# Kernel tuning notes

Hardware: AMD Instinct MI355X
Metric: run time of the kernel (lower is better)

## Reference

```python
import jax, jax.numpy as jnp
import numpy as np
from jax.scipy.special import gammaln

# ---- constants matching init_kwargs ----
D = 64            # num_nodes
K = 64            # DiBS latent rank (k = d default)
P = 32            # n_particles
N_MC = 16         # MC graph samples for score-function grad estimator
PROJ = 128        # proj_dims
N = 2048          # observations
H = 5.0           # h_latent (Frobenius squared-exponential kernel bandwidth)
ALPHA = 0.2       # alpha_linear * t  (single SVGD step)
STEP = 0.005      # SVGD step size
ALPHA_MU = 1.0
ALPHA_LAMBD = float(D + 2)
THETA_MU = 0.0
P_EDGE = 4.0 / (D - 1)          # Erdos-Renyi edge prob (~2 expected edges/node)
LATENT_STD = 1.0 / np.sqrt(K)   # DiBS default latent prior std


def bge_log_marginal(g, data, mu0, alpha_mu, alpha_lambd):
    """BGe log marginal likelihood log p(data | G) for 0/1 adjacency g [d,d]."""
    n, d = data.shape
    small_t = alpha_mu * (alpha_lambd - d - 1.0) / (alpha_mu + 1.0)
    xbar = data.mean(0)
    xc = data - xbar
    R = small_t * jnp.eye(d) + xc.T @ xc \
        + (n * alpha_mu / (n + alpha_mu)) * jnp.outer(xbar - mu0, xbar - mu0)

    def masked_slogdet(mask):  # logdet of R restricted to mask-selected rows/cols
        m = jnp.outer(mask, mask)
        return jnp.linalg.slogdet(m * R + (1.0 - m) * jnp.eye(d))[1]

    def node_score(j):
        parents = g[:, j].astype(R.dtype)
        pj = jnp.maximum(parents, (jnp.arange(d) == j).astype(R.dtype))
        l = jnp.sum(parents)
        log_gamma = (0.5 * (jnp.log(alpha_mu) - jnp.log(n + alpha_mu))
                     + gammaln(0.5 * (n + alpha_lambd - d + l + 1.0))
                     - gammaln(0.5 * (alpha_lambd - d + l + 1.0))
                     - 0.5 * n * jnp.log(jnp.pi)
                     + 0.5 * (alpha_lambd - d + 2.0 * l + 1.0) * jnp.log(small_t))
        return (log_gamma
                + 0.5 * (n + alpha_lambd - d + l) * masked_slogdet(parents)
                - 0.5 * (n + alpha_lambd - d + l + 1.0) * masked_slogdet(pj))

    return jnp.sum(jax.vmap(node_score)(jnp.arange(d)))


def _dense(key, fan_in, fan_out):
    return jax.random.normal(key, (fan_in, fan_out), jnp.float32) * 0.05


def setup_inputs() -> dict:
    key = jax.random.key(0)
    ks = jax.random.split(key, 16)
    return {
        "z_gt": jax.random.normal(ks[0], (N, D), jnp.float32),
        "init_particles_z": jax.random.normal(ks[1], (P, D, K, 2), jnp.float32) * LATENT_STD,
        "enc_w0": _dense(ks[2], D * D, 20), "enc_b0": jnp.zeros(20, jnp.float32),
        "enc_w1": _dense(ks[3], 20, D),     "enc_b1": jnp.zeros(D, jnp.float32),
        "enc_w2": _dense(ks[4], D, D),      "enc_b2": jnp.zeros(D, jnp.float32),
        "mu_w0": _dense(ks[5], D, D), "mu_b0": jnp.zeros(D, jnp.float32),
        "mu_w1": _dense(ks[6], D, D), "mu_b1": jnp.zeros(D, jnp.float32),
        "lv_w0": _dense(ks[7], D, D), "lv_b0": jnp.zeros(D, jnp.float32),
        "lv_w1": _dense(ks[8], D, D), "lv_b1": jnp.zeros(D, jnp.float32),
        "dec_w0": _dense(ks[9], D, 10),       "dec_b0": jnp.zeros(10, jnp.float32),
        "dec_w1": _dense(ks[10], 10, PROJ),   "dec_b1": jnp.zeros(PROJ, jnp.float32),
        "dec_w2": _dense(ks[11], PROJ, PROJ), "dec_b2": jnp.zeros(PROJ, jnp.float32),
        "seed": 0,
    }


def reference(z_gt, init_particles_z, enc_w0, enc_b0, enc_w1, enc_b1, enc_w2, enc_b2,
              mu_w0, mu_b0, mu_w1, mu_b1, lv_w0, lv_b0, lv_w1, lv_b1,
              dec_w0, dec_b0, dec_w1, dec_b1, dec_w2, dec_b2, seed):
    key = jax.random.key(seed)
    d = z_gt.shape[1]
    od = 1.0 - jnp.eye(d)
    z = init_particles_z                                   # [P,d,k,2]
    u, v = z[..., 0], z[..., 1]
    scores = jnp.einsum('pik,pjk->pij', u, v)              # [P,d,d]
    probs = jax.nn.sigmoid(ALPHA * scores) * od            # soft graph, zero diag

    # --- score-function estimate of grad_z log E_G[p(data|G)] (DiBS marginal) ---
    key, sk = jax.random.split(key)
    gs = jax.random.bernoulli(sk, probs[:, None], (P, N_MC, d, d)).astype(z.dtype) * od
    mu0_inf = jnp.zeros(d, z.dtype)
    logp = jax.vmap(jax.vmap(
        lambda g: bge_log_marginal(g, z_gt, mu0_inf, 1.0, d + 2.0)))(gs)   # [P,S]
    w = jax.nn.softmax(logp, axis=1)                       # self-normalized weights
    M = ALPHA * (gs - probs[:, None]) * od                 # d log q(G|Z) / d scores
    grad_u = jnp.einsum('ps,psij,pjk->pik', w, M, v)
    grad_v = jnp.einsum('ps,psij,pik->pjk', w, M, u)

    # --- grad of soft-graph ER prior + Gaussian latent prior ---
    logit_pe = jnp.log(P_EDGE) - jnp.log1p(-P_EDGE)
    Mp = ALPHA * probs * (1.0 - probs) * logit_pe * od
    grad_u = grad_u + jnp.einsum('pij,pjk->pik', Mp, v) - u / (LATENT_STD ** 2)
    grad_v = grad_v + jnp.einsum('pij,pik->pjk', Mp, u) - v / (LATENT_STD ** 2)
    grads = jnp.stack([grad_u, grad_v], axis=-1)           # [P,d,k,2]

    # --- one SVGD step with Frobenius squared-exponential kernel ---
    zf = z.reshape(P, -1)
    gf = grads.reshape(P, -1)
    sq = jnp.sum((zf[:, None] - zf[None]) ** 2, -1)
    Kmat = jnp.exp(-sq / H)                                # symmetric [P,P]
    rep = (-2.0 / H) * (Kmat @ zf - zf * Kmat.sum(1, keepdims=True))
    z_new = z + STEP * ((Kmat @ gf + rep) / P).reshape(z.shape)

    # --- hard graphs: particle_to_g_lim (alpha -> inf) ---
    s2 = jnp.einsum('pik,pjk->pij', z_new[..., 0], z_new[..., 1])
    g_hard = (s2 > 0).astype(z.dtype) * od                 # [P,d,d]

    mu0_bge = jnp.full(d, THETA_MU, z.dtype)
    log_p_z_given_g = jax.vmap(
        lambda g: bge_log_marginal(g, z_gt, mu0_bge, ALPHA_MU, ALPHA_LAMBD))(g_hard)

    # --- q(z | G) encoder (batched over particles) ---
    gf2 = g_hard.reshape(g_hard.shape[0], d * d)
    h = jax.nn.relu(gf2 @ enc_w0 + enc_b0)
    h = jax.nn.relu(h @ enc_w1 + enc_b1)
    h = jax.nn.relu(h @ enc_w2 + enc_b2)
    q_mu = jax.nn.relu(h @ mu_w0 + mu_b0) @ mu_w1 + mu_b1
    q_lv = jax.nn.relu(h @ lv_w0 + lv_b0) @ lv_w1 + lv_b1

    key, rk = jax.random.split(key)
    eps = jax.random.normal(rk, q_lv.shape, q_lv.dtype)
    q_z = q_mu + eps * jnp.exp(0.5 * q_lv)                 # reparameterize

    # --- decoder ---
    hdec = jax.nn.relu(q_z @ dec_w0 + dec_b0)
    hdec = jax.nn.relu(hdec @ dec_w1 + dec_b1)
    recons = hdec @ dec_w2 + dec_b2                        # [P, PROJ]

    return recons, log_p_z_given_g, q_z, q_mu, q_lv, g_hard, z_new
```

## Files before the change

kernel.cpp:

```cpp
#include <hip/hip_runtime.h>
#include <stdint.h>
#include <math.h>

typedef unsigned long long u64;
typedef unsigned int u32;
typedef unsigned short u16;

#define C_P 32
#define C_S 16
#define C_D 64
#define C_N 2048

#define R_OFF      0
#define CTAB_OFF   4160
#define KEYS_OFF   4224
#define PROBS_OFF  4232
#define GROW_OFF   135304
#define GCOL_OFF   168072
#define NS_OFF     200840
#define W_OFF      233608
#define GF_OFF     234120
#define KM_OFF     365192
#define ZN_OFF     365704
#define NS2_OFF    496776

#define WL_LIST0 16

#define HBLK 768
#define TB1 1280
#define TB0 2112
#define TB2 1312
#define E_H  (HBLK)
#define E_1  (E_H + TB1)
#define E_0  (E_1 + TB0)
#define NBLK_ALL (E_0 + TB2)

#define O_REC   0
#define O_LOGP  4096
#define O_QZ    4128
#define O_QMU   6176
#define O_QLV   8224
#define O_GH    10272
#define O_ZN    141344
#define O_TOTAL 403488

__device__ __forceinline__ void tf2x32(u32 k0, u32 k1, u32 x0, u32 x1,
                                       u32& o0, u32& o1) {
  u32 ks2 = k0 ^ k1 ^ 0x1BD11BDAu;
  x0 += k0; x1 += k1;
#define TFR(r) { x0 += x1; x1 = (x1 << r) | (x1 >> (32 - r)); x1 ^= x0; }
  TFR(13) TFR(15) TFR(26) TFR(6)   x0 += k1;  x1 += ks2 + 1u;
  TFR(17) TFR(29) TFR(16) TFR(24)  x0 += ks2; x1 += k0 + 2u;
  TFR(13) TFR(15) TFR(26) TFR(6)   x0 += k0;  x1 += k1 + 3u;
  TFR(17) TFR(29) TFR(16) TFR(24)  x0 += k1;  x1 += ks2 + 4u;
  TFR(13) TFR(15) TFR(26) TFR(6)   x0 += ks2; x1 += k0 + 5u;
#undef TFR
  o0 = x0; o1 = x1;
}

__device__ __forceinline__ double d_erfinv(double x) {
  double w = -log1p(-x * x);
  double p;
  if (w < 5.0) {
    w -= 2.5;
    p = 2.81022636e-08;
    p = 3.43273939e-07  + p * w;
    p = -3.5233877e-06  + p * w;
    p = -4.39150654e-06 + p * w;
    p = 0.00021858087   + p * w;
    p = -0.00125372503  + p * w;
    p = -0.00417768164  + p * w;
    p = 0.246640727     + p * w;
    p = 1.50140941      + p * w;
  } else {
    w = sqrt(w) - 3.0;
    p = -0.000200214257;
    p = 0.000100950558  + p * w;
    p = 0.00134934322   + p * w;
    p = -0.00367342844  + p * w;
    p = 0.00573950773   + p * w;
    p = -0.0076224613   + p * w;
    p = 0.00943887047   + p * w;
    p = 1.00167406      + p * w;
    p = 2.83297682      + p * w;
  }
  return p * x;
}

__device__ __forceinline__ double stirl(double z) {
  double zi = 1.0 / z;
  double zi2 = zi * zi;
  double s = (z - 0.5) * log(z) - z + 0.9189385332046727;
  s += zi * (1.0 / 12.0 - zi2 * (1.0 / 360.0 - zi2 * (1.0 / 1260.0)));
  return s;
}

__global__ void k_R(const float* x, double* ws, const int* seedp) {
  __shared__ double pS[8][64], pX[8][64];
  __shared__ double xbar[64];
  int j = blockIdx.x, t = threadIdx.x;
  int i = t & 63, c = t >> 6;
  if (j == 0) {
    if (t < 64) {
      int l = t;
      double term = (l >= 2) ? log((2049.0 + (double)l) / (4.0 * (1.0 + (double)l)))
                             : 0.0;
      double v = term;
#pragma unroll
      for (int off = 2; off <= 32; off <<= 1) {
        double o = __shfl_up(v, off, 64);
        if (l >= off) v += o;
      }
      const double LOG_HALF = -0.6931471805599453;
      double c0 = -0.5 * log(2049.0)
                - 1024.0 * log(3.14159265358979323846);
      double seed = (l & 1)
        ? c0 + stirl(1026.0) + 2.5 * LOG_HALF
        : c0 + stirl(1025.5) + 0.12078223763524522235 + 1.5 * LOG_HALF;
      ws[CTAB_OFF + l] = seed + v;
    }
    if (t < 8) ((u32*)(ws + GF_OFF))[t] = 0;
    if (t == 0) {
      u32 kk0 = 0u, kk1 = (u32)seedp[0];
      u32 a0, a1, s0, s1, r0, r1, d0, d1;
      tf2x32(kk0, kk1, 0u, 0u, a0, a1);
      tf2x32(kk0, kk1, 0u, 1u, s0, s1);
      tf2x32(a0, a1, 0u, 0u, d0, d1); (void)d0; (void)d1;
      tf2x32(a0, a1, 0u, 1u, r0, r1);
      u32* keys = (u32*)(ws + KEYS_OFF);
      keys[0] = s0; keys[1] = s1; keys[2] = r0; keys[3] = r1;
    }
  }
  double sx = 0.0, sxx = 0.0;
  for (int n = c * 256; n < (c + 1) * 256; n++) {
    double xi = (double)x[n * 64 + i];
    double xj = (double)x[n * 64 + j];
    sx += xi; sxx += xi * xj;
  }
  pS[c][i] = sx; pX[c][i] = sxx;
  __syncthreads();
  if (t < 64) {
    double S = 0.0, X = 0.0;
    for (int cc = 0; cc < 8; cc++) { S += pS[cc][i]; X += pX[cc][i]; }
    xbar[i] = S / 2048.0;
    pX[0][i] = X;
  }
  __syncthreads();
  if (t < 64) {
    double xbi = xbar[i], xbj = xbar[j];
    double s = pX[0][i] - 2048.0 * xbi * xbj + (2048.0 / 2049.0) * xbi * xbj;
    if (i == j) s += 0.5;
    ((float*)(ws + R_OFF))[i * 64 + j] = (float)s;
  }
}

__global__ __launch_bounds__(64) void k_probs(const float* z, double* ws) {
  float* probs = (float*)(ws + PROBS_OFF);
  int b = blockIdx.x; int p = b >> 6, i = b & 63;
  int j = threadIdx.x;
  __shared__ float V[64 * 65];
  __shared__ float us[64];
  int k = j;
  us[k] = z[((p * 64 + i) * 64 + k) * 2 + 0];
  for (int jj = 0; jj < 64; jj++)
    V[jj * 65 + k] = z[((p * 64 + jj) * 64 + k) * 2 + 1];
  __syncthreads();
  float s = 0.f;
  for (int kk = 0; kk < 64; kk++)
    s += us[kk] * V[j * 65 + kk];
  float pr = (i == j) ? 0.f : 1.f / (1.f + expf(-0.2f * s));
  probs[(p * 64 + i) * 64 + j] = pr;
}

__global__ void k_sample(double* ws) {
  const float* probs = (const float*)(ws + PROBS_OFF);
  const u32* keys = (const u32*)(ws + KEYS_OFF);
  u64* grow = (u64*)(ws + GROW_OFF);
  u64* gcol = (u64*)(ws + GCOL_OFF);
  u32* wl = (u32*)(ws + GF_OFF);
  int ps = blockIdx.x;
  int p = ps >> 4;
  int j = threadIdx.x;
  u32 k0 = keys[0], k1 = keys[1];
  u64 colmask = 0;
  for (int i = 0; i < 64; i++) {
    u32 lin = (u32)(ps * 4096 + i * 64 + j);
    u32 o0, o1; tf2x32(k0, k1, 0u, lin, o0, o1);
    u32 bits = o0 ^ o1;
    float f = __uint_as_float((bits >> 9) | 0x3f800000u) - 1.0f;
    bool bit = (f < probs[(p * 64 + i) * 64 + j]);
    u64 rm = __ballot(bit);
    if (j == 0) grow[ps * 64 + i] = rm;
    if (bit) colmask |= (1ull << i);
  }
  gcol[ps * 64 + j] = colmask;
  int m = (int)__popcll(colmask) + 1;
  int tier = (m <= 32) ? 0 : (m <= 36) ? 1 : (m <= 40) ? 2 : 3;
#pragma unroll
  for (int t = 0; t < 4; t++) {
    u64 b = __ballot(tier == t);
    if (tier == t) {
      int leader = (int)__builtin_ctzll(b);
      u32 off = (u32)__popcll(b & ((1ull << j) - 1ull));
      u32 base = 0;
      if (j == leader) base = atomicAdd(&wl[t], (u32)__popcll(b));
      base = (u32)__shfl((int)base, leader, 64);
      wl[WL_LIST0 + t * 32768 + base + off] = (u32)(ps * 64 + j);
    }
  }
}

__device__ __forceinline__ float rdlane(float x, int l) {
  return __uint_as_float(__builtin_amdgcn_readlane(__float_as_uint(x), (u32)l));
}

template<int MMAX>
__device__ __forceinline__ void tier_body2(const float* Rf, const double* ctab,
                                           const u64* masks, double* nodescore,
                                           const u32* wl, int tier,
                                           u32 brel, u32 nb, int (*idx)[2][64]) {
  int w = threadIdx.x >> 6;
  int lane = threadIdx.x & 63;
  u32 cnt = wl[tier];
  const u32* list = wl + WL_LIST0 + tier * 32768;
  u32 npair = (cnt + 1) >> 1;
  for (u32 ti = brel * 4 + (u32)w; ti < npair; ti += nb * 4) {
    u32 iA = 2 * ti, iB = iA + 1;
    bool hasB = (iB < cnt);
    int taskA = (int)list[iA];
    int taskB = (int)list[hasB ? iB : iA];
    u64 maskA = masks[taskA];
    u64 maskB = masks[taskB];
    int PA = (int)__popcll(maskA), PB = (int)__popcll(maskB);
    idx[w][0][lane] = 0;
    idx[w][1][lane] = 0;
    __builtin_amdgcn_wave_barrier();
    {
      u64 belowA = maskA & ((1ull << lane) - 1ull);
      if ((maskA >> lane) & 1ull) idx[w][0][(int)__popcll(belowA)] = lane;
      if (lane == 0) idx[w][0][PA] = taskA & 63;
      u64 belowB = maskB & ((1ull << lane) - 1ull);
      if ((maskB >> lane) & 1ull) idx[w][1][(int)__popcll(belowB)] = lane;
      if (lane == 0) idx[w][1][PB] = taskB & 63;
    }
    __builtin_amdgcn_wave_barrier();
    int rowA = idx[w][0][lane];
    int rowB = idx[w][1][lane];
    float va[MMAX], vb[MMAX];
#pragma unroll
    for (int c = 0; c < MMAX; c++) {
      va[c] = Rf[idx[w][0][c] * 64 + rowA];
      vb[c] = Rf[idx[w][1][c] * 64 + rowB];
    }
    float pivA = 1.0f, pivB = 1.0f;
#pragma unroll
    for (int k = 0; k < MMAX; k++) {
      float dkA = rdlane(va[k], k);
      float dkB = rdlane(vb[k], k);
      if (lane == k) { pivA = dkA; pivB = dkB; }
      float nsA = -va[k] * __builtin_amdgcn_rcpf(dkA);
      float nsB = -vb[k] * __builtin_amdgcn_rcpf(dkB);
#pragma unroll
      for (int b2 = k + 1; b2 < MMAX; b2++) {
        va[b2] += nsA * rdlane(va[k], b2);
        vb[b2] += nsB * rdlane(vb[k], b2);
      }
    }
    {
      int mA = PA + 1;
      float lastd = __shfl(pivA, PA, 64);
      float lv = (lane < mA) ? __logf(pivA) : 0.f;
      for (int off = 32; off > 0; off >>= 1) lv += __shfl_down(lv, off, 64);
      if (lane == 0) {
        double l = (double)PA;
        nodescore[taskA] = ctab[PA]
                         - 0.5 * (2050.0 + l) * (double)__logf(lastd)
                         - 0.5 * (double)lv;
      }
    }
    if (hasB) {
      int mB = PB + 1;
      float lastd = __shfl(pivB, PB, 64);
      float lv = (lane < mB) ? __logf(pivB) : 0.f;
      for (int off = 32; off > 0; off >>= 1) lv += __shfl_down(lv, off, 64);
      if (lane == 0) {
        double l = (double)PB;
        nodescore[taskB] = ctab[PB]
                         - 0.5 * (2050.0 + l) * (double)__logf(lastd)
                         - 0.5 * (double)lv;
      }
    }
    __builtin_amdgcn_wave_barrier();
  }
}

template<int MMAX>
__device__ __forceinline__ void tier_body(const float* Rf, const double* ctab,
                                          const u64* masks, double* nodescore,
                                          const u32* wl, int tier,
                                          u32 brel, u32 nb, int (*idx)[64]) {
  int w = threadIdx.x >> 6;
  int lane = threadIdx.x & 63;
  u32 cnt = wl[tier];
  const u32* list = wl + WL_LIST0 + tier * 32768;
  for (u32 ti = brel * 4 + (u32)w; ti < cnt; ti += nb * 4) {
    int task = (int)list[ti];
    int j = task & 63;
    u64 mask = masks[task];
    int P = (int)__popcll(mask);
    int m = P + 1;
    idx[w][lane] = 0;
    __builtin_amdgcn_wave_barrier();
    u64 below = mask & ((1ull << lane) - 1ull);
    if ((mask >> lane) & 1ull) idx[w][(int)__popcll(below)] = lane;
    if (lane == 0) idx[w][P] = j;
    __builtin_amdgcn_wave_barrier();
    int myrow = idx[w][lane];
    float v[MMAX];
#pragma unroll
    for (int c = 0; c < MMAX; c++)
      v[c] = Rf[idx[w][c] * 64 + myrow];
    float mypiv = 1.0f;
#pragma unroll
    for (int k = 0; k < MMAX; k++) {
      if (k < m) {
        float dk = rdlane(v[k], k);
        if (lane == k) mypiv = dk;
        float ns = -v[k] * __builtin_amdgcn_rcpf(dk);
#pragma unroll
        for (int b = k + 1; b < MMAX; b++)
          v[b] += ns * rdlane(v[k], b);
      }
    }
    float lastd = __shfl(mypiv, P, 64);
    float lv = (lane < m) ? __logf(mypiv) : 0.f;
    for (int off = 32; off > 0; off >>= 1) lv += __shfl_down(lv, off, 64);
    if (lane == 0) {
      double l = (double)P;
      nodescore[task] = ctab[P]
                      - 0.5 * (2050.0 + l) * (double)__logf(lastd)
                      - 0.5 * (double)lv;
    }
    __builtin_amdgcn_wave_barrier();
  }
}

#define WB() __builtin_amdgcn_wave_barrier()

__device__ void heavy_body(const float* Rf, const double* ctab,
                           const u64* masks, double* nodescore,
                           const u32* wl, u32 brel, u32 nb,
                           float* T, int* idx) {
  if (threadIdx.x >= 64) return;
  int lane = threadIdx.x;
  u32 cnt = wl[3];
  const u32* list = wl + WL_LIST0 + 3 * 32768;
  for (u32 ii = brel; ii < cnt; ii += nb) {
    WB();
    int task = (int)list[ii];
    int j = task & 63;
    u64 mask = masks[task];
    int P = (int)__popcll(mask);
    int m = P + 1;
    u64 below = mask & ((1ull << lane) - 1ull);
    if ((mask >> lane) & 1ull) idx[(int)__popcll(below)] = lane;
    if (lane == 0) idx[P] = j;
    WB();
    int trLane = (lane * (lane + 1)) >> 1;
    if (lane < m) {
      int cidx = idx[lane];
      int tr = 0;
      for (int r = 0; r < m; r++) {
        if (lane <= r) T[tr + lane] = Rf[idx[r] * 64 + cidx];
        tr += r + 1;
      }
    }
    WB();
    float mypiv = 1.0f, lastd = 1.0f;
    float v[40];
#pragma unroll
    for (int c = 0; c < 40; c++)
      v[c] = T[trLane + c];
#pragma unroll
    for (int k = 0; k < 40; k++) {
      if (k < m) {
        float dk = rdlane(v[k], k);
        if (lane == k) mypiv = dk;
        lastd = dk;
        float ns = -v[k] * __builtin_amdgcn_rcpf(dk);
#pragma unroll
        for (int b = k + 1; b < 40; b++)
          v[b] += ns * rdlane(v[k], b);
      }
    }
    if (m > 40) {
      for (int b = 40; b < m; b++) {
        float acc = 0.f;
#pragma unroll
        for (int k = 0; k < 40; k++) {
          float dk = rdlane(v[k], k);
          float abk = rdlane(v[k], b);
          acc += v[k] * abk * __builtin_amdgcn_rcpf(dk);
        }
        if (lane >= b) T[trLane + b] -= acc;
      }
      WB();
      for (int k = 40; k < m; k++) {
        float dk = T[((k * (k + 1)) >> 1) + k];
        if (lane == k) mypiv = dk;
        lastd = dk;
        float sk = T[trLane + k] * __builtin_amdgcn_rcpf(dk);
        for (int b = k + 1; b < m; b++) {
          float abk = T[((b * (b + 1)) >> 1) + k];
          if (lane >= b) T[trLane + b] -= sk * abk;
        }
        WB();
      }
    }
    double vv = (lane < m) ? log((double)mypiv) : 0.0;
    for (int off = 32; off > 0; off >>= 1) vv += __shfl_down(vv, off, 64);
    if (lane == 0) {
      double logB = vv;
      double logA = logB - log((double)lastd);
      double l = (double)P;
      nodescore[task] = ctab[P]
                      + 0.5 * (2050.0 + l) * logA
                      - 0.5 * (2051.0 + l) * logB;
    }
  }
}

__global__ __launch_bounds__(256) void k_chol_all(const float* Rf, const double* ctab,
                                                  const u64* masks, double* nodescore,
                                                  const u32* wl) {
  __shared__ int idx2[4][2][64];
  __shared__ int idx4[4][64];
  __shared__ float T[2080];
  __shared__ int idxh[64];
  u32 b = blockIdx.x;
  if (b < E_H)      heavy_body(Rf, ctab, masks, nodescore, wl, b, HBLK, T, idxh);
  else if (b < E_1) tier_body2<36>(Rf, ctab, masks, nodescore, wl, 1, b - E_H, TB1, idx2);
  else if (b < E_0) tier_body2<32>(Rf, ctab, masks, nodescore, wl, 0, b - E_1, TB0, idx2);
  else              tier_body<40>(Rf, ctab, masks, nodescore, wl, 2, b - E_0, TB2, idx4);
}

template<bool TRANSPOSE>
__global__ __launch_bounds__(64) void k_chol(const float* Rf, const double* ctab,
                                             const u64* masks, double* nodescore) {
  __shared__ float T[2080];
  __shared__ int idx[64];
  int task = blockIdx.x;
  int j = task & 63;
  int lane = threadIdx.x;
  u64 mask;
  if (TRANSPOSE) {
    int p = task >> 6;
    u64 rm = masks[p * 64 + lane];
    mask = __ballot((rm >> j) & 1ull);
  } else {
    mask = masks[task];
  }
  int P = (int)__popcll(mask);
  int m = P + 1;
  u64 below = mask & ((1ull << lane) - 1ull);
  if ((mask >> lane) & 1ull) idx[(int)__popcll(below)] = lane;
  if (lane == 0) idx[P] = j;
  __syncthreads();
  int trLane = (lane * (lane + 1)) >> 1;
  if (lane < m) {
    int cidx = idx[lane];
    int tr = 0;
    for (int r = 0; r < m; r++) {
      if (lane <= r) T[tr + lane] = Rf[idx[r] * 64 + cidx];
      tr += r + 1;
    }
  }
  __syncthreads();
  float mypiv = 1.0f, lastd = 1.0f;
  float v[40];
#pragma unroll
  for (int c = 0; c < 40; c++)
    v[c] = T[trLane + c];
#pragma unroll
  for (int k = 0; k < 40; k++) {
    if (k < m) {
      float dk = rdlane(v[k], k);
      if (lane == k) mypiv = dk;
      lastd = dk;
      float ns = -v[k] * __builtin_amdgcn_rcpf(dk);
#pragma unroll
      for (int b = k + 1; b < 40; b++)
        v[b] += ns * rdlane(v[k], b);
    }
  }
  if (m > 40) {
    for (int b = 40; b < m; b++) {
      float acc = 0.f;
#pragma unroll
      for (int k = 0; k < 40; k++) {
        float dk = rdlane(v[k], k);
        float abk = rdlane(v[k], b);
        acc += v[k] * abk * __builtin_amdgcn_rcpf(dk);
      }
      if (lane >= b) T[trLane + b] -= acc;
    }
    __syncthreads();
    for (int k = 40; k < m; k++) {
      float dk = T[((k * (k + 1)) >> 1) + k];
      if (lane == k) mypiv = dk;
      lastd = dk;
      float sk = T[trLane + k] * __builtin_amdgcn_rcpf(dk);
      for (int b = k + 1; b < m; b++) {
        float abk = T[((b * (b + 1)) >> 1) + k];
        if (lane >= b) T[trLane + b] -= sk * abk;
      }
      __syncthreads();
    }
  }
  double vv = (lane < m) ? log((double)mypiv) : 0.0;
  for (int off = 32; off > 0; off >>= 1) vv += __shfl_down(vv, off, 64);
  if (lane == 0) {
    double logB = vv;
    double logA = logB - log((double)lastd);
    double l = (double)P;
    nodescore[task] = ctab[P]
                    + 0.5 * (2050.0 + l) * logA
                    - 0.5 * (2051.0 + l) * logB;
  }
}

__global__ void k_logpw(const double* ns, double* w) {
  int p = blockIdx.x, t = threadIdx.x;
  __shared__ double part[64];
  int s = t & 15, c = t >> 4;
  double acc = 0.0;
  for (int j = c * 16; j < (c + 1) * 16; j++)
    acc += ns[(p * 16 + s) * 64 + j];
  part[t] = acc;
  __syncthreads();
  if (t < 16) part[t] = part[t] + part[t + 16] + part[t + 32] + part[t + 48];
  __syncthreads();
  if (t == 0) {
    double m = part[0];
    for (int s2 = 1; s2 < 16; s2++) m = fmax(m, part[s2]);
    double e[16], sum = 0.0;
    for (int s2 = 0; s2 < 16; s2++) { e[s2] = exp(part[s2] - m); sum += e[s2]; }
    for (int s2 = 0; s2 < 16; s2++) w[p * 16 + s2] = e[s2] / sum;
  }
}

__global__ void k_grad(double* ws, const float* z) {
  const float* probs = (const float*)(ws + PROBS_OFF);
  const double* w = ws + W_OFF;
  const u64* grow = (const u64*)(ws + GROW_OFF);
  const u64* gcol = (const u64*)(ws + GCOL_OFF);
  float* gf = (float*)(ws + GF_OFF);
  const float LOGIT = -2.6903717578966254f;
  int bb = blockIdx.x;
  int k = threadIdx.x;
  __shared__ float acc[64];
  if (bb < 2048) {
    int p = bb >> 6, i = bb & 63;
    float gb = 0.f, wsum = 0.f;
    for (int s = 0; s < 16; s++) {
      float wv = (float)w[p * 16 + s];
      wsum += wv;
      gb += wv * (float)((grow[(p * 16 + s) * 64 + i] >> k) & 1ull);
    }
    float pr = probs[(p * 64 + i) * 64 + k];
    float od = (i == k) ? 0.f : 1.f;
    acc[k] = (0.2f * (gb - pr * wsum) + 0.2f * pr * (1.f - pr) * LOGIT) * od;
    __syncthreads();
    float s = 0.f;
    for (int j = 0; j < 64; j++)
      s += acc[j] * z[((p * 64 + j) * 64 + k) * 2 + 1];
    s -= 64.f * z[((p * 64 + i) * 64 + k) * 2 + 0];
    gf[p * 8192 + (i * 64 + k) * 2 + 0] = s;
  } else if (bb < 4096) {
    int b = bb - 2048;
    int p = b >> 6, j = b & 63;
    float gb = 0.f, wsum = 0.f;
    for (int s = 0; s < 16; s++) {
      float wv = (float)w[p * 16 + s];
      wsum += wv;
      gb += wv * (float)((gcol[(p * 16 + s) * 64 + j] >> k) & 1ull);
    }
    float pr = probs[(p * 64 + k) * 64 + j];
    float od = (k == j) ? 0.f : 1.f;
    acc[k] = (0.2f * (gb - pr * wsum) + 0.2f * pr * (1.f - pr) * LOGIT) * od;
    __syncthreads();
    float s = 0.f;
    for (int i = 0; i < 64; i++)
      s += acc[i] * z[((p * 64 + i) * 64 + k) * 2 + 0];
    s -= 64.f * z[((p * 64 + j) * 64 + k) * 2 + 1];
    gf[p * 8192 + (j * 64 + k) * 2 + 1] = s;
  } else {
    float* Km = (float*)(ws + KM_OFF);
    int b = bb - 4096;
    int a = b >> 5, b2 = b & 31;
    float accf = 0.f;
    for (int d0 = k; d0 < 8192; d0 += 64) {
      float diff = z[a * 8192 + d0] - z[b2 * 8192 + d0];
      accf += diff * diff;
    }
    for (int off = 32; off > 0; off >>= 1) accf += __shfl_down(accf, off, 64);
    if (k == 0) Km[a * 32 + b2] = expf(-accf / 5.0f);
  }
}

__global__ void k_znew(const float* z, double* ws, float* out) {
  const float* Km = (const float*)(ws + KM_OFF);
  const float* gf = (const float*)(ws + GF_OFF);
  float* zn = (float*)(ws + ZN_OFF);
  int gid = blockIdx.x * 64 + threadIdx.x;
  int p = gid >> 13, t = gid & 8191;
  float zp = z[p * 8192 + t];
  float accg = 0.f, accz = 0.f, ks = 0.f;
  for (int b = 0; b < 32; b++) {
    float kv = Km[p * 32 + b];
    accg += kv * gf[b * 8192 + t];
    accz += kv * z[b * 8192 + t];
    ks += kv;
  }
  float rep = -0.4f * (accz - zp * ks);
  float v = zp + 0.005f * ((accg + rep) / 32.f);
  zn[p * 8192 + t] = v;
  out[O_ZN + p * 8192 + t] = v;
}

__global__ __launch_bounds__(64) void k_s2col(double* ws, float* out) {
  const float* zn = (const float*)(ws + ZN_OFF);
  u64* grow2 = (u64*)(ws + NS_OFF);
  int b = blockIdx.x; int p = b >> 6, i = b & 63;
  int j = threadIdx.x;
  __shared__ float V[64 * 65];
  __shared__ float us[64];
  int k = j;
  us[k] = zn[p * 8192 + (i * 64 + k) * 2 + 0];
  for (int jj = 0; jj < 64; jj++)
    V[jj * 65 + k] = zn[p * 8192 + (jj * 64 + k) * 2 + 1];
  __syncthreads();
  float s = 0.f;
  for (int kk = 0; kk < 64; kk++)
    s += us[kk] * V[j * 65 + kk];
  bool bit = (i != j) && (s > 0.0f);
  out[O_GH + (p * 64 + i) * 64 + j] = bit ? 1.0f : 0.0f;
  u64 m = __ballot(bit);
  if (j == 0) grow2[p * 64 + i] = m;
}

__global__ __launch_bounds__(256) void k_mlp(double* ws, float* out, const double* ns2,
    const float* ew0, const float* eb0, const float* ew1, const float* eb1,
    const float* ew2, const float* eb2,
    const float* mw0, const float* mb0, const float* mw1, const float* mb1,
    const float* lw0, const float* lb0, const float* lw1, const float* lb1,
    const float* dw0, const float* db0, const float* dw1, const float* db1,
    const float* dw2, const float* db2) {
  int p = blockIdx.x, t = threadIdx.x;
  int w = t >> 6, lane = t & 63;
  const u64* grow2 = (const u64*)(ws + NS_OFF);
  const u32* keys = (const u32*)(ws + KEYS_OFF);
  __shared__ float pt[4][64];
  __shared__ float e0p[4][20];
  __shared__ float h0[20], h1[64], h2[64], hm[64], hl[64];
  __shared__ float qmu[64], qlv[64], qz[64], h3[10], h4[128];

  if (w == 0) {
    double vv = ns2[p * 64 + lane];
    for (int off = 32; off > 0; off >>= 1) vv += __shfl_down(vv, off, 64);
    if (lane == 0) out[O_LOGP + p] = (float)vv;
  }

  {
    int i = t >> 2;
    int jb = (t & 3) * 16;
    u32 m16 = (u32)((grow2[p * 64 + i] >> jb) & 0xFFFFull);
    float acc[20];
#pragma unroll
    for (int o = 0; o < 20; o++) acc[o] = 0.f;
    const float4* wb = (const float4*)(ew0 + (size_t)(t * 16) * 20);
#pragma unroll
    for (int q = 0; q < 16; q++) {
      float mq = (float)((m16 >> q) & 1u);
      float4 r0 = wb[q * 5 + 0], r1 = wb[q * 5 + 1], r2 = wb[q * 5 + 2];
      float4 r3 = wb[q * 5 + 3], r4 = wb[q * 5 + 4];
      acc[0]  += mq * r0.x; acc[1]  += mq * r0.y; acc[2]  += mq * r0.z; acc[3]  += mq * r0.w;
      acc[4]  += mq * r1.x; acc[5]  += mq * r1.y; acc[6]  += mq * r1.z; acc[7]  += mq * r1.w;
      acc[8]  += mq * r2.x; acc[9]  += mq * r2.y; acc[10] += mq * r2.z; acc[11] += mq * r2.w;
      acc[12] += mq * r3.x; acc[13] += mq * r3.y; acc[14] += mq * r3.z; acc[15] += mq * r3.w;
      acc[16] += mq * r4.x; acc[17] += mq * r4.y; acc[18] += mq * r4.z; acc[19] += mq * r4.w;
    }
#pragma unroll
    for (int o = 0; o < 20; o++) {
      float v = acc[o];
      for (int off = 32; off > 0; off >>= 1) v += __shfl_down(v, off, 64);
      if (lane == 0) e0p[w][o] = v;
    }
  }
  __syncthreads();
  if (t < 20)
    h0[t] = fmaxf(eb0[t] + e0p[0][t] + e0p[1][t] + e0p[2][t] + e0p[3][t], 0.f);
  __syncthreads();

  {
    float s = 0.f;
#pragma unroll
    for (int q = 0; q < 5; q++) s += h0[w * 5 + q] * ew1[(w * 5 + q) * 64 + lane];
    pt[w][lane] = s;
  }
  __syncthreads();
  if (w == 0)
    h1[lane] = fmaxf(eb1[lane] + pt[0][lane] + pt[1][lane] + pt[2][lane] + pt[3][lane], 0.f);
  __syncthreads();

  {
    float s = 0.f;
#pragma unroll
    for (int q = 0; q < 16; q++) s += h1[w * 16 + q] * ew2[(w * 16 + q) * 64 + lane];
    pt[w][lane] = s;
  }
  __syncthreads();
  if (w == 0)
    h2[lane] = fmaxf(eb2[lane] + pt[0][lane] + pt[1][lane] + pt[2][lane] + pt[3][lane], 0.f);
  __syncthreads();

  {
    const float* W = (w < 2) ? mw0 : lw0;
    int qb = (w & 1) * 32;
    float s = 0.f;
#pragma unroll
    for (int q = 0; q < 32; q++) s += h2[qb + q] * W[(qb + q) * 64 + lane];
    pt[w][lane] = s;
  }
  __syncthreads();
  if (w == 0) hm[lane] = fmaxf(mb0[lane] + pt[0][lane] + pt[1][lane], 0.f);
  if (w == 1) hl[lane] = fmaxf(lb0[lane] + pt[2][lane] + pt[3][lane], 0.f);
  __syncthreads();

  {
    const float* W = (w < 2) ? mw1 : lw1;
    const float* src = (w < 2) ? hm : hl;
    int qb = (w & 1) * 32;
    float s = 0.f;
#pragma unroll
    for (int q = 0; q < 32; q++) s += src[qb + q] * W[(qb + q) * 64 + lane];
    pt[w][lane] = s;
  }
  __syncthreads();
  if (w == 0) qmu[lane] = mb1[lane] + pt[0][lane] + pt[1][lane];
  if (w == 1) qlv[lane] = lb1[lane] + pt[2][lane] + pt[3][lane];
  __syncthreads();

  if (w == 0) {
    u32 o0, o1;
    tf2x32(keys[2], keys[3], 0u, (u32)(p * 64 + lane), o0, o1);
    u32 bits = o0 ^ o1;
    float f = __uint_as_float((bits >> 9) | 0x3f800000u) - 1.0f;
    float LOF = __uint_as_float(0xBF7FFFFFu);
    float uu = fmaxf(LOF, f * 2.0f + LOF);
    float eps = (float)(1.4142135623730951 * d_erfinv((double)uu));
    float qzv = qmu[lane] + eps * expf(0.5f * qlv[lane]);
    qz[lane] = qzv;
    out[O_QZ  + p * 64 + lane] = qzv;
    out[O_QMU + p * 64 + lane] = qmu[lane];
    out[O_QLV + p * 64 + lane] = qlv[lane];
  }
  __syncthreads();

  {
    float s = 0.f;
    if (lane < 10) {
#pragma unroll
      for (int q = 0; q < 16; q++) s += qz[w * 16 + q] * dw0[(w * 16 + q) * 10 + lane];
    }
    pt[w][lane] = s;
  }
  __syncthreads();
  if (w == 0 && lane < 10)
    h3[lane] = fmaxf(db0[lane] + pt[0][lane] + pt[1][lane] + pt[2][lane] + pt[3][lane], 0.f);
  __syncthreads();

  {
    int o = (w >> 1) * 64 + lane;
    int qb = (w & 1) * 5;
    float s = 0.f;
#pragma unroll
    for (int q = 0; q < 5; q++) s += h3[qb + q] * dw1[(qb + q) * 128 + o];
    pt[w][lane] = s;
  }
  __syncthreads();
  if (w == 0) h4[lane]      = fmaxf(db1[lane]      + pt[0][lane] + pt[1][lane], 0.f);
  if (w == 1) h4[64 + lane] = fmaxf(db1[64 + lane] + pt[2][lane] + pt[3][lane], 0.f);
  __syncthreads();

  {
    int o = (w >> 1) * 64 + lane;
    int qb = (w & 1) * 64;
    float s = 0.f;
#pragma unroll
    for (int q = 0; q < 64; q++) s += h4[qb + q] * dw2[(qb + q) * 128 + o];
    pt[w][lane] = s;
  }
  __syncthreads();
  if (w == 0) out[O_REC + p * 128 + lane]      = db2[lane]      + pt[0][lane] + pt[1][lane];
  if (w == 1) out[O_REC + p * 128 + 64 + lane] = db2[64 + lane] + pt[2][lane] + pt[3][lane];
}

extern "C" void kernel_launch(void* const* d_in, const int* in_sizes, int n_in,
                              void* d_out, int out_size, void* d_ws, size_t ws_size,
                              hipStream_t stream) {
  (void)in_sizes; (void)n_in; (void)out_size; (void)ws_size;
  const float* z_gt = (const float*)d_in[0];
  const float* z0   = (const float*)d_in[1];
  const float* ew0 = (const float*)d_in[2];  const float* eb0 = (const float*)d_in[3];
  const float* ew1 = (const float*)d_in[4];  const float* eb1 = (const float*)d_in[5];
  const float* ew2 = (const float*)d_in[6];  const float* eb2 = (const float*)d_in[7];
  const float* mw0 = (const float*)d_in[8];  const float* mb0 = (const float*)d_in[9];
  const float* mw1 = (const float*)d_in[10]; const float* mb1 = (const float*)d_in[11];
  const float* lw0 = (const float*)d_in[12]; const float* lb0 = (const float*)d_in[13];
  const float* lw1 = (const float*)d_in[14]; const float* lb1 = (const float*)d_in[15];
  const float* dw0 = (const float*)d_in[16]; const float* db0 = (const float*)d_in[17];
  const float* dw1 = (const float*)d_in[18]; const float* db1 = (const float*)d_in[19];
  const float* dw2 = (const float*)d_in[20]; const float* db2 = (const float*)d_in[21];
  const int* seed = (const int*)d_in[22];
  double* ws = (double*)d_ws;
  float* out = (float*)d_out;
  const float* Rf = (const float*)(ws + R_OFF);
  const u32* wl = (const u32*)(ws + GF_OFF);

  k_R<<<64, 512, 0, stream>>>(z_gt, ws, seed);
  k_probs<<<C_P * C_D, 64, 0, stream>>>(z0, ws);
  k_sample<<<C_P * C_S, 64, 0, stream>>>(ws);
  k_chol_all<<<NBLK_ALL, 256, 0, stream>>>(Rf, ws + CTAB_OFF,
      (const u64*)(ws + GCOL_OFF), ws + NS_OFF, wl);
  k_logpw<<<C_P, 64, 0, stream>>>(ws + NS_OFF, ws + W_OFF);
  k_grad<<<2 * C_P * C_D + C_P * C_P, 64, 0, stream>>>(ws, z0);
  k_znew<<<(C_P * 8192) / 64, 64, 0, stream>>>(z0, ws, out);
  k_s2col<<<C_P * C_D, 64, 0, stream>>>(ws, out);
  k_chol<true><<<C_P * C_D, 64, 0, stream>>>(Rf, ws + CTAB_OFF,
      (const u64*)(ws + NS_OFF), ws + NS2_OFF);
  k_mlp<<<C_P, 256, 0, stream>>>(ws, out, ws + NS2_OFF,
      ew0, eb0, ew1, eb1, ew2, eb2,
      mw0, mb0, mw1, mb1, lw0, lb0, lw1, lb1,
      dw0, db0, dw1, db1, dw2, db2);
}
```

Measured before the change: 336.5 us.

## Fuse R and probs kernels, and fold softmax weights into grad kernel

Merges k_R and k_probs into one k_init launch with 320 blocks of 512 threads. The probs half now computes 8 rows per block and shares the V tile across them. Removes the k_logpw launch by recomputing each particle's log-weight softmax inside every k_grad block. This cuts two kernel launches and the gaps between them. In exchange, every grad block redundantly reads 1024 node scores and runs a serial softmax.

```diff
diff --git a/kernel.cpp b/kernel.cpp
--- a/kernel.cpp
+++ b/kernel.cpp
@@ -95,81 +95,83 @@
   return s;
 }
 
-__global__ void k_R(const float* x, double* ws, const int* seedp) {
-  __shared__ double pS[8][64], pX[8][64];
-  __shared__ double xbar[64];
-  int j = blockIdx.x, t = threadIdx.x;
-  int i = t & 63, c = t >> 6;
-  if (j == 0) {
+__global__ void k_init(const float* x, const float* z, double* ws, const int* seedp) {
+  int t = threadIdx.x;
+  if (blockIdx.x < 64) {
+    __shared__ double pS[8][64], pX[8][64];
+    __shared__ double xbar[64];
+    int j = blockIdx.x;
+    int i = t & 63, c = t >> 6;
+    if (j == 0) {
+      if (t < 64) {
+        int l = t;
+        double term = (l >= 2) ? log((2049.0 + (double)l) / (4.0 * (1.0 + (double)l)))
+                               : 0.0;
+        double v = term;
+#pragma unroll
+        for (int off = 2; off <= 32; off <<= 1) {
+          double o = __shfl_up(v, off, 64);
+          if (l >= off) v += o;
+        }
+        const double LOG_HALF = -0.6931471805599453;
+        double c0 = -0.5 * log(2049.0)
+                  - 1024.0 * log(3.14159265358979323846);
+        double seed = (l & 1)
+          ? c0 + stirl(1026.0) + 2.5 * LOG_HALF
+          : c0 + stirl(1025.5) + 0.12078223763524522235 + 1.5 * LOG_HALF;
+        ws[CTAB_OFF + l] = seed + v;
+      }
+      if (t < 8) ((u32*)(ws + GF_OFF))[t] = 0;
+      if (t == 0) {
+        u32 kk0 = 0u, kk1 = (u32)seedp[0];
+        u32 a0, a1, s0, s1, r0, r1, d0, d1;
+        tf2x32(kk0, kk1, 0u, 0u, a0, a1);
+        tf2x32(kk0, kk1, 0u, 1u, s0, s1);
+        tf2x32(a0, a1, 0u, 0u, d0, d1); (void)d0; (void)d1;
+        tf2x32(a0, a1, 0u, 1u, r0, r1);
+        u32* keys = (u32*)(ws + KEYS_OFF);
+        keys[0] = s0; keys[1] = s1; keys[2] = r0; keys[3] = r1;
+      }
+    }
+    double sx = 0.0, sxx = 0.0;
+    for (int n = c * 256; n < (c + 1) * 256; n++) {
+      double xi = (double)x[n * 64 + i];
+      double xj = (double)x[n * 64 + j];
+      sx += xi; sxx += xi * xj;
+    }
+    pS[c][i] = sx; pX[c][i] = sxx;
+    __syncthreads();
     if (t < 64) {
-      int l = t;
-      double term = (l >= 2) ? log((2049.0 + (double)l) / (4.0 * (1.0 + (double)l)))
-                             : 0.0;
-      double v = term;
-#pragma unroll
-      for (int off = 2; off <= 32; off <<= 1) {
-        double o = __shfl_up(v, off, 64);
-        if (l >= off) v += o;
-      }
-      const double LOG_HALF = -0.6931471805599453;
-      double c0 = -0.5 * log(2049.0)
-                - 1024.0 * log(3.14159265358979323846);
-      double seed = (l & 1)
-        ? c0 + stirl(1026.0) + 2.5 * LOG_HALF
-        : c0 + stirl(1025.5) + 0.12078223763524522235 + 1.5 * LOG_HALF;
-      ws[CTAB_OFF + l] = seed + v;
-    }
-    if (t < 8) ((u32*)(ws + GF_OFF))[t] = 0;
-    if (t == 0) {
-      u32 kk0 = 0u, kk1 = (u32)seedp[0];
-      u32 a0, a1, s0, s1, r0, r1, d0, d1;
-      tf2x32(kk0, kk1, 0u, 0u, a0, a1);
-      tf2x32(kk0, kk1, 0u, 1u, s0, s1);
-      tf2x32(a0, a1, 0u, 0u, d0, d1); (void)d0; (void)d1;
-      tf2x32(a0, a1, 0u, 1u, r0, r1);
-      u32* keys = (u32*)(ws + KEYS_OFF);
-      keys[0] = s0; keys[1] = s1; keys[2] = r0; keys[3] = r1;
-    }
-  }
-  double sx = 0.0, sxx = 0.0;
-  for (int n = c * 256; n < (c + 1) * 256; n++) {
-    double xi = (double)x[n * 64 + i];
-    double xj = (double)x[n * 64 + j];
-    sx += xi; sxx += xi * xj;
-  }
-  pS[c][i] = sx; pX[c][i] = sxx;
-  __syncthreads();
-  if (t < 64) {
-    double S = 0.0, X = 0.0;
-    for (int cc = 0; cc < 8; cc++) { S += pS[cc][i]; X += pX[cc][i]; }
-    xbar[i] = S / 2048.0;
-    pX[0][i] = X;
-  }
-  __syncthreads();
-  if (t < 64) {
-    double xbi = xbar[i], xbj = xbar[j];
-    double s = pX[0][i] - 2048.0 * xbi * xbj + (2048.0 / 2049.0) * xbi * xbj;
-    if (i == j) s += 0.5;
-    ((float*)(ws + R_OFF))[i * 64 + j] = (float)s;
-  }
-}
-
-__global__ __launch_bounds__(64) void k_probs(const float* z, double* ws) {
-  float* probs = (float*)(ws + PROBS_OFF);
-  int b = blockIdx.x; int p = b >> 6, i = b & 63;
-  int j = threadIdx.x;
-  __shared__ float V[64 * 65];
-  __shared__ float us[64];
-  int k = j;
-  us[k] = z[((p * 64 + i) * 64 + k) * 2 + 0];
-  for (int jj = 0; jj < 64; jj++)
-    V[jj * 65 + k] = z[((p * 64 + jj) * 64 + k) * 2 + 1];
-  __syncthreads();
-  float s = 0.f;
-  for (int kk = 0; kk < 64; kk++)
-    s += us[kk] * V[j * 65 + kk];
-  float pr = (i == j) ? 0.f : 1.f / (1.f + expf(-0.2f * s));
-  probs[(p * 64 + i) * 64 + j] = pr;
+      double S = 0.0, X = 0.0;
+      for (int cc = 0; cc < 8; cc++) { S += pS[cc][i]; X += pX[cc][i]; }
+      xbar[i] = S / 2048.0;
+      pX[0][i] = X;
+    }
+    __syncthreads();
+    if (t < 64) {
+      double xbi = xbar[i], xbj = xbar[j];
+      double s = pX[0][i] - 2048.0 * xbi * xbj + (2048.0 / 2049.0) * xbi * xbj;
+      if (i == j) s += 0.5;
+      ((float*)(ws + R_OFF))[i * 64 + j] = (float)s;
+    }
+  } else {
+    __shared__ float V[64 * 65];
+    __shared__ float us[8][64];
+    float* probs = (float*)(ws + PROBS_OFF);
+    int b2 = blockIdx.x - 64;
+    int p = b2 >> 3;
+    int i = (b2 & 7) * 8 + (t >> 6);
+    int j = t & 63, w = t >> 6;
+    for (int jj = w; jj < 64; jj += 8)
+      V[jj * 65 + j] = z[((p * 64 + jj) * 64 + j) * 2 + 1];
+    us[w][j] = z[((p * 64 + i) * 64 + j) * 2 + 0];
+    __syncthreads();
+    float s = 0.f;
+    for (int kk = 0; kk < 64; kk++)
+      s += us[w][kk] * V[j * 65 + kk];
+    float pr = (i == j) ? 0.f : 1.f / (1.f + expf(-0.2f * s));
+    probs[(p * 64 + i) * 64 + j] = pr;
+  }
 }
 
 __global__ void k_sample(double* ws) {
@@ -529,71 +531,73 @@
   }
 }
 
-__global__ void k_logpw(const double* ns, double* w) {
-  int p = blockIdx.x, t = threadIdx.x;
-  __shared__ double part[64];
-  int s = t & 15, c = t >> 4;
-  double acc = 0.0;
-  for (int j = c * 16; j < (c + 1) * 16; j++)
-    acc += ns[(p * 16 + s) * 64 + j];
-  part[t] = acc;
-  __syncthreads();
-  if (t < 16) part[t] = part[t] + part[t + 16] + part[t + 32] + part[t + 48];
-  __syncthreads();
-  if (t == 0) {
-    double m = part[0];
-    for (int s2 = 1; s2 < 16; s2++) m = fmax(m, part[s2]);
-    double e[16], sum = 0.0;
-    for (int s2 = 0; s2 < 16; s2++) { e[s2] = exp(part[s2] - m); sum += e[s2]; }
-    for (int s2 = 0; s2 < 16; s2++) w[p * 16 + s2] = e[s2] / sum;
-  }
-}
-
 __global__ void k_grad(double* ws, const float* z) {
   const float* probs = (const float*)(ws + PROBS_OFF);
-  const double* w = ws + W_OFF;
   const u64* grow = (const u64*)(ws + GROW_OFF);
   const u64* gcol = (const u64*)(ws + GCOL_OFF);
+  const double* ns = ws + NS_OFF;
   float* gf = (float*)(ws + GF_OFF);
   const float LOGIT = -2.6903717578966254f;
   int bb = blockIdx.x;
   int k = threadIdx.x;
   __shared__ float acc[64];
-  if (bb < 2048) {
-    int p = bb >> 6, i = bb & 63;
-    float gb = 0.f, wsum = 0.f;
-    for (int s = 0; s < 16; s++) {
-      float wv = (float)w[p * 16 + s];
-      wsum += wv;
-      gb += wv * (float)((grow[(p * 16 + s) * 64 + i] >> k) & 1ull);
-    }
-    float pr = probs[(p * 64 + i) * 64 + k];
-    float od = (i == k) ? 0.f : 1.f;
-    acc[k] = (0.2f * (gb - pr * wsum) + 0.2f * pr * (1.f - pr) * LOGIT) * od;
-    __syncthreads();
-    float s = 0.f;
-    for (int j = 0; j < 64; j++)
-      s += acc[j] * z[((p * 64 + j) * 64 + k) * 2 + 1];
-    s -= 64.f * z[((p * 64 + i) * 64 + k) * 2 + 0];
-    gf[p * 8192 + (i * 64 + k) * 2 + 0] = s;
-  } else if (bb < 4096) {
-    int b = bb - 2048;
-    int p = b >> 6, j = b & 63;
-    float gb = 0.f, wsum = 0.f;
-    for (int s = 0; s < 16; s++) {
-      float wv = (float)w[p * 16 + s];
-      wsum += wv;
-      gb += wv * (float)((gcol[(p * 16 + s) * 64 + j] >> k) & 1ull);
-    }
-    float pr = probs[(p * 64 + k) * 64 + j];
-    float od = (k == j) ? 0.f : 1.f;
-    acc[k] = (0.2f * (gb - pr * wsum) + 0.2f * pr * (1.f - pr) * LOGIT) * od;
-    __syncthreads();
-    float s = 0.f;
-    for (int i = 0; i < 64; i++)
-      s += acc[i] * z[((p * 64 + i) * 64 + k) * 2 + 0];
-    s -= 64.f * z[((p * 64 + j) * 64 + k) * 2 + 1];
-    gf[p * 8192 + (j * 64 + k) * 2 + 1] = s;
+  __shared__ double part[64];
+  __shared__ double wsh[16];
+  if (bb < 4096) {
+    int p = (bb < 2048) ? (bb >> 6) : ((bb - 2048) >> 6);
+    {
+      int s = k & 15, c = k >> 4;
+      double a2 = 0.0;
+      for (int j2 = c * 16; j2 < (c + 1) * 16; j2++)
+        a2 += ns[(p * 16 + s) * 64 + j2];
+      part[k] = a2;
+      __syncthreads();
+      if (k < 16) part[k] = part[k] + part[k + 16] + part[k + 32] + part[k + 48];
+      __syncthreads();
+      if (k == 0) {
+        double m2 = part[0];
+        for (int s2 = 1; s2 < 16; s2++) m2 = fmax(m2, part[s2]);
+        double e[16], sum = 0.0;
+        for (int s2 = 0; s2 < 16; s2++) { e[s2] = exp(part[s2] - m2); sum += e[s2]; }
+        for (int s2 = 0; s2 < 16; s2++) wsh[s2] = e[s2] / sum;
+      }
+      __syncthreads();
+    }
+    if (bb < 2048) {
+      int i = bb & 63;
+      float gb = 0.f, wsum = 0.f;
+      for (int s = 0; s < 16; s++) {
+        float wv = (float)wsh[s];
+        wsum += wv;
+        gb += wv * (float)((grow[(p * 16 + s) * 64 + i] >> k) & 1ull);
+      }
+      float pr = probs[(p * 64 + i) * 64 + k];
+      float od = (i == k) ? 0.f : 1.f;
+      acc[k] = (0.2f * (gb - pr * wsum) + 0.2f * pr * (1.f - pr) * LOGIT) * od;
+      __syncthreads();
+      float s = 0.f;
+      for (int j = 0; j < 64; j++)
+        s += acc[j] * z[((p * 64 + j) * 64 + k) * 2 + 1];
+      s -= 64.f * z[((p * 64 + i) * 64 + k) * 2 + 0];
+      gf[p * 8192 + (i * 64 + k) * 2 + 0] = s;
+    } else {
+      int j = (bb - 2048) & 63;
+      float gb = 0.f, wsum = 0.f;
+      for (int s = 0; s < 16; s++) {
+        float wv = (float)wsh[s];
+        wsum += wv;
+        gb += wv * (float)((gcol[(p * 16 + s) * 64 + j] >> k) & 1ull);
+      }
+      float pr = probs[(p * 64 + k) * 64 + j];
+      float od = (k == j) ? 0.f : 1.f;
+      acc[k] = (0.2f * (gb - pr * wsum) + 0.2f * pr * (1.f - pr) * LOGIT) * od;
+      __syncthreads();
+      float s = 0.f;
+      for (int i = 0; i < 64; i++)
+        s += acc[i] * z[((p * 64 + i) * 64 + k) * 2 + 0];
+      s -= 64.f * z[((p * 64 + j) * 64 + k) * 2 + 1];
+      gf[p * 8192 + (j * 64 + k) * 2 + 1] = s;
+    }
   } else {
     float* Km = (float*)(ws + KM_OFF);
     int b = bb - 4096;
@@ -828,12 +832,10 @@
   const float* Rf = (const float*)(ws + R_OFF);
   const u32* wl = (const u32*)(ws + GF_OFF);
 
-  k_R<<<64, 512, 0, stream>>>(z_gt, ws, seed);
-  k_probs<<<C_P * C_D, 64, 0, stream>>>(z0, ws);
+  k_init<<<320, 512, 0, stream>>>(z_gt, z0, ws, seed);
   k_sample<<<C_P * C_S, 64, 0, stream>>>(ws);
   k_chol_all<<<NBLK_ALL, 256, 0, stream>>>(Rf, ws + CTAB_OFF,
       (const u64*)(ws + GCOL_OFF), ws + NS_OFF, wl);
-  k_logpw<<<C_P, 64, 0, stream>>>(ws + NS_OFF, ws + W_OFF);
   k_grad<<<2 * C_P * C_D + C_P * C_P, 64, 0, stream>>>(ws, z0);
   k_znew<<<(C_P * 8192) / 64, 64, 0, stream>>>(z0, ws, out);
   k_s2col<<<C_P * C_D, 64, 0, stream>>>(ws, out);
```

Measured after the change: 329.3 us. 1.02x faster.
